# Kernel optimization log

Measured on AMD Instinct MI355X. Metric: run time of the kernel, lower is better.

The kernel has to match this reference:

```python
import jax, jax.numpy as jnp
import numpy as np

N = 50000
E = 1_600_000
IN_CH = 128
HEADS = 4
OUT_CH = 32
NEG_SLOPE = 0.2


def setup_inputs() -> dict:
    key = jax.random.key(0)
    k1, k2, k3, k4, k5, k6 = jax.random.split(key, 6)
    x = jax.random.normal(k1, (N, IN_CH), dtype=jnp.float32)
    edge_index = jax.random.randint(k2, (2, E), 0, N, dtype=jnp.int64)
    # GATConv params: linear weight, per-head attention vectors, output bias
    scale = 1.0 / np.sqrt(IN_CH)
    W = jax.random.normal(k3, (IN_CH, HEADS * OUT_CH), dtype=jnp.float32) * scale
    att_src = jax.random.normal(k4, (HEADS, OUT_CH), dtype=jnp.float32) * scale
    att_dst = jax.random.normal(k5, (HEADS, OUT_CH), dtype=jnp.float32) * scale
    bias = jnp.zeros((HEADS * OUT_CH,), dtype=jnp.float32)
    return {"x": x, "edge_index": edge_index, "W": W, "att_src": att_src,
            "att_dst": att_dst, "bias": bias}


def reference(x, edge_index, W, att_src, att_dst, bias):
    n = x.shape[0]
    # add self loops (PyG GATConv default add_self_loops=True)
    loops = jnp.arange(n, dtype=edge_index.dtype)
    src = jnp.concatenate([edge_index[0], loops])  # message source j
    dst = jnp.concatenate([edge_index[1], loops])  # message target i

    h = (x @ W).reshape(n, HEADS, OUT_CH)  # [N,H,C]
    a_src = jnp.einsum('nhc,hc->nh', h, att_src)  # [N,H]
    a_dst = jnp.einsum('nhc,hc->nh', h, att_dst)  # [N,H]

    e = jax.nn.leaky_relu(a_src[src] + a_dst[dst], NEG_SLOPE)  # [E+N,H]
    # segment softmax over incoming edges of each target node
    m = jax.ops.segment_max(e, dst, num_segments=n)  # [N,H]
    p = jnp.exp(e - m[dst])
    s = jax.ops.segment_sum(p, dst, num_segments=n)  # [N,H]
    alpha = p / s[dst]  # self loops guarantee s > 0

    # weighted scatter-aggregate of source features
    out = jax.ops.segment_sum(alpha[:, :, None] * h[src], dst, num_segments=n)  # [N,H,C]
    out = out.reshape(n, HEADS * OUT_CH) + bias
    return jax.nn.elu(out)
```

## Files before the change

kernel.cpp:

```cpp
#include <hip/hip_runtime.h>
#include <hip/hip_bf16.h>

#define IN_CH 128
#define HEADS 4
#define OUT_CH 32
#define HC 128
#define NEG_SLOPE 0.2f
#define BSHIFT 6
#define CHUNK 4096
#define BUCKCAP 2816

typedef __attribute__((ext_vector_type(8))) short bf16x8;
typedef __attribute__((ext_vector_type(4))) float f32x4;

__device__ __forceinline__ unsigned short f2bf(float f) {
  unsigned int u = __float_as_uint(f);
  return (unsigned short)((u + 0x7fffu + ((u >> 16) & 1u)) >> 16);
}
__device__ __forceinline__ float bf2f(unsigned short b) {
  return __uint_as_float(((unsigned int)b) << 16);
}
__device__ __forceinline__ float bflo(unsigned int g) {
  return __uint_as_float((g & 0xffffu) << 16);
}
__device__ __forceinline__ float bfhi(unsigned int g) {
  return __uint_as_float(g & 0xffff0000u);
}

__global__ void zero_i32(int* __restrict__ p, int n) {
  int i = blockIdx.x * blockDim.x + threadIdx.x;
  if (i < n) p[i] = 0;
}

__global__ void cvt_params(const void* __restrict__ Wr, const void* __restrict__ asr,
                           const void* __restrict__ adr, const void* __restrict__ br,
                           const void* __restrict__ xptr, const void* __restrict__ eptr,
                           float* __restrict__ Wf, unsigned short* __restrict__ Wtb,
                           float* __restrict__ asf,
                           float* __restrict__ adf, float* __restrict__ bf,
                           int* __restrict__ cursorA, int* __restrict__ flags) {
  __shared__ int sok[256], sz[256];
  int t = threadIdx.x;
  {
    const unsigned short* u = (const unsigned short*)xptr;
    float a = fabsf(bf2f(u[t]));
    sok[t] = (a >= 1e-6f && a <= 1e3f) ? 1 : 0;
    const int* ip = (const int*)eptr;
    int z = 0;
#pragma unroll
    for (int k = 0; k < 4; k++) z += (ip[2 * (t * 4 + k) + 1] == 0) ? 1 : 0;
    sz[t] = z;
    __syncthreads();
    for (int s = 128; s > 0; s >>= 1) {
      if (t < s) { sok[t] += sok[t + s]; sz[t] += sz[t + s]; }
      __syncthreads();
    }
  }
  int isbf = (sok[0] >= 240) ? 1 : 0;
  int is64 = (sz[0] >= 900) ? 1 : 0;
  if (blockIdx.x == 0 && t == 0) { flags[0] = isbf; flags[1] = is64; }

  int i = blockIdx.x * blockDim.x + t;
  auto rd = [&](const void* p, int k) -> float {
    return isbf ? bf2f(((const unsigned short*)p)[k]) : ((const float*)p)[k];
  };
  if (i < 1024) cursorA[i] = i * BUCKCAP;
  if (i < IN_CH * HC) {
    float v = rd(Wr, i);
    Wf[i] = v;
    int r = i >> 7, c = i & 127;
    Wtb[c * IN_CH + r] = f2bf(v);
  } else {
    int r = i - IN_CH * HC;
    if (r < HC)            asf[r] = rd(asr, r);
    else if (r < 2 * HC)   adf[r - HC] = rd(adr, r - HC);
    else if (r < 3 * HC)   bf[r - 2 * HC] = rd(br, r - 2 * HC);
  }
}

__device__ __forceinline__ void load_edge(const void* __restrict__ ei,
                                          const int* __restrict__ flags,
                                          int e, int E, int& j, int& d) {
  if (flags[1]) {
    const long long* q = (const long long*)ei;
    j = (int)q[e]; d = (int)q[E + e];
  } else {
    const int* p = (const int*)ei;
    j = p[e]; d = p[E + e];
  }
}

__device__ void gemm_body(const void* __restrict__ xraw, const float* __restrict__ W,
                          const float* __restrict__ asf, const float* __restrict__ adf,
                          unsigned short* __restrict__ h_bf,
                          float* __restrict__ a_srcO, float* __restrict__ a_dstO,
                          int N, int isbf, float (*xs)[33], int bid) {
  int t = threadIdx.x;
  int nb = bid * 32;
  for (int r = 0; r < 16; r++) {
    int idx = r * 256 + t;
    int nl = idx >> 7;
    int c = idx & 127;
    int n = nb + nl;
    float v = 0.f;
    if (n < N) {
      size_t gi = (size_t)n * IN_CH + c;
      v = isbf ? bf2f(((const unsigned short*)xraw)[gi]) : ((const float*)xraw)[gi];
    }
    xs[c][nl] = v;
  }
  __syncthreads();
  int tc = t & 31, c0 = tc * 4;
  int tn = t >> 5, n0 = tn * 4;
  float acc[4][4];
#pragma unroll
  for (int i = 0; i < 4; i++)
#pragma unroll
    for (int q = 0; q < 4; q++) acc[i][q] = 0.f;
  for (int k = 0; k < 128; k++) {
    float4 w = *(const float4*)&W[k * HC + c0];
    float x0 = xs[k][n0], x1 = xs[k][n0 + 1], x2 = xs[k][n0 + 2], x3 = xs[k][n0 + 3];
    acc[0][0] += x0 * w.x; acc[0][1] += x0 * w.y; acc[0][2] += x0 * w.z; acc[0][3] += x0 * w.w;
    acc[1][0] += x1 * w.x; acc[1][1] += x1 * w.y; acc[1][2] += x1 * w.z; acc[1][3] += x1 * w.w;
    acc[2][0] += x2 * w.x; acc[2][1] += x2 * w.y; acc[2][2] += x2 * w.z; acc[2][3] += x2 * w.w;
    acc[3][0] += x3 * w.x; acc[3][1] += x3 * w.y; acc[3][2] += x3 * w.z; acc[3][3] += x3 * w.w;
  }
#pragma unroll
  for (int i = 0; i < 4; i++) {
    int n = nb + n0 + i;
    if (n >= N) continue;
    size_t o = (size_t)n * HC + c0;
    ushort4 hb;
    hb.x = f2bf(acc[i][0]);
    hb.y = f2bf(acc[i][1]);
    hb.z = f2bf(acc[i][2]);
    hb.w = f2bf(acc[i][3]);
    *(ushort4*)&h_bf[o] = hb;
  }
  float4 wsc = *(const float4*)&asf[c0];
  float4 wdc = *(const float4*)&adf[c0];
  int hh = tc >> 3;
#pragma unroll
  for (int i = 0; i < 4; i++) {
    float ps = acc[i][0] * wsc.x + acc[i][1] * wsc.y + acc[i][2] * wsc.z + acc[i][3] * wsc.w;
    float pd = acc[i][0] * wdc.x + acc[i][1] * wdc.y + acc[i][2] * wdc.z + acc[i][3] * wdc.w;
    ps += __shfl_xor(ps, 1, 64); ps += __shfl_xor(ps, 2, 64); ps += __shfl_xor(ps, 4, 64);
    pd += __shfl_xor(pd, 1, 64); pd += __shfl_xor(pd, 2, 64); pd += __shfl_xor(pd, 4, 64);
    int n = nb + n0 + i;
    if ((tc & 7) == 0 && n < N) {
      a_srcO[n * HEADS + hh] = ps;
      a_dstO[n * HEADS + hh] = pd;
    }
  }
}

__device__ void gemm_mfma_body(const unsigned short* __restrict__ xb,
                               const unsigned short* __restrict__ Wtb,
                               const float* __restrict__ asf, const float* __restrict__ adf,
                               unsigned short* __restrict__ h_bf,
                               float* __restrict__ a_srcO, float* __restrict__ a_dstO,
                               int N, int bid) {
  int t = threadIdx.x;
  int w = t >> 6, l = t & 63;
  int lr = l & 15, lk = l >> 4;
  int nb = bid * 32;
  int node_base = nb + (w & 1) * 16;
  int ch0 = (w >> 1) * 64;
  int arow = node_base + lr;
  if (arow >= N) arow = N - 1;
  const unsigned short* xrow = xb + (size_t)arow * IN_CH + lk * 8;

  f32x4 acc[4];
#pragma unroll
  for (int ct = 0; ct < 4; ct++) acc[ct] = (f32x4){0.f, 0.f, 0.f, 0.f};

#pragma unroll
  for (int ks = 0; ks < 4; ks++) {
    bf16x8 afrag = *(const bf16x8*)(xrow + ks * 32);
#pragma unroll
    for (int ct = 0; ct < 4; ct++) {
      const unsigned short* wrow =
          Wtb + (size_t)(ch0 + ct * 16 + lr) * IN_CH + ks * 32 + lk * 8;
      bf16x8 bfrag = *(const bf16x8*)wrow;
      acc[ct] = __builtin_amdgcn_mfma_f32_16x16x32_bf16(afrag, bfrag, acc[ct], 0, 0, 0);
    }
  }

  float ps[4][2], pd[4][2];
#pragma unroll
  for (int i = 0; i < 4; i++) { ps[i][0] = ps[i][1] = pd[i][0] = pd[i][1] = 0.f; }
#pragma unroll
  for (int ct = 0; ct < 4; ct++) {
    int col = ch0 + ct * 16 + lr;
    float as_c = asf[col], ad_c = adf[col];
    int hw = ct >> 1;
#pragma unroll
    for (int i = 0; i < 4; i++) {
      float v = acc[ct][i];
      int row = node_base + lk * 4 + i;
      if (row < N) h_bf[(size_t)row * HC + col] = f2bf(v);
      ps[i][hw] += v * as_c;
      pd[i][hw] += v * ad_c;
    }
  }
#pragma unroll
  for (int i = 0; i < 4; i++) {
#pragma unroll
    for (int hw = 0; hw < 2; hw++) {
      float s = ps[i][hw], d2 = pd[i][hw];
      s += __shfl_xor(s, 1, 64); s += __shfl_xor(s, 2, 64);
      s += __shfl_xor(s, 4, 64); s += __shfl_xor(s, 8, 64);
      d2 += __shfl_xor(d2, 1, 64); d2 += __shfl_xor(d2, 2, 64);
      d2 += __shfl_xor(d2, 4, 64); d2 += __shfl_xor(d2, 8, 64);
      int row = node_base + lk * 4 + i;
      if (lr == 0 && row < N) {
        int hh = (ch0 >> 5) + hw;
        a_srcO[row * HEADS + hh] = s;
        a_dstO[row * HEADS + hh] = d2;
      }
    }
  }
}

__device__ void partA_body(const void* __restrict__ ei, int* __restrict__ cursorA,
                           unsigned int* __restrict__ ebuf, int E, int N,
                           const int* __restrict__ flags, int* hist, int bid) {
  int nbuck = (N + ((1 << BSHIFT) - 1)) >> BSHIFT;
  int t = threadIdx.x;
  for (int b = t; b < nbuck; b += 256) hist[b] = 0;
  __syncthreads();
  int base = bid * CHUNK;
  unsigned int v[16];
#pragma unroll
  for (int k = 0; k < 16; k++) {
    int e = base + k * 256 + t;
    if (e < E) {
      int j, d;
      load_edge(ei, flags, e, E, j, d);
      v[k] = (unsigned int)j | ((unsigned int)d << 16);
      atomicAdd(&hist[d >> BSHIFT], 1);
    } else v[k] = 0xffffffffu;
  }
  __syncthreads();
  for (int b = t; b < nbuck; b += 256) {
    int c = hist[b];
    if (c > 0) hist[b] = atomicAdd(&cursorA[b], c);
  }
  __syncthreads();
#pragma unroll
  for (int k = 0; k < 16; k++) {
    if (v[k] != 0xffffffffu) {
      int b = (int)(v[k] >> 16) >> BSHIFT;
      int pos = atomicAdd(&hist[b], 1);
      if (pos < (b + 1) * BUCKCAP) ebuf[pos] = v[k];
    }
  }
}

__global__ void fused_gemm_partA(const void* __restrict__ xraw, const float* __restrict__ W,
                                 const unsigned short* __restrict__ Wtb,
                                 const float* __restrict__ asf, const float* __restrict__ adf,
                                 unsigned short* __restrict__ h_bf,
                                 float* __restrict__ a_src, float* __restrict__ a_dst,
                                 const void* __restrict__ ei, int* __restrict__ cursorA,
                                 unsigned int* __restrict__ ebuf, int E, int N,
                                 const int* __restrict__ flags, int NB_G) {
  __shared__ __align__(16) char smem[16896];
  if (blockIdx.x < NB_G) {
    if (flags[0]) {
      gemm_mfma_body((const unsigned short*)xraw, Wtb, asf, adf, h_bf,
                     a_src, a_dst, N, blockIdx.x);
    } else {
      gemm_body(xraw, W, asf, adf, h_bf, a_src, a_dst, N, 0,
                (float(*)[33])smem, blockIdx.x);
    }
  } else {
    partA_body(ei, cursorA, ebuf, E, N, flags, (int*)smem, blockIdx.x - NB_G);
  }
}

__global__ void gemm_kernel(const void* __restrict__ xraw, const float* __restrict__ W,
                            const unsigned short* __restrict__ Wtb,
                            const float* __restrict__ asf, const float* __restrict__ adf,
                            unsigned short* __restrict__ h_bf,
                            float* __restrict__ a_src, float* __restrict__ a_dst,
                            int N, const int* __restrict__ flags) {
  __shared__ float xs[128][33];
  if (flags[0]) {
    gemm_mfma_body((const unsigned short*)xraw, Wtb, asf, adf, h_bf,
                   a_src, a_dst, N, blockIdx.x);
  } else {
    gemm_body(xraw, W, asf, adf, h_bf, a_src, a_dst, N, 0, xs, blockIdx.x);
  }
}

__global__ void partB(const unsigned int* __restrict__ ebuf, const int* __restrict__ cursorA,
                      int* __restrict__ rowbeg, int* __restrict__ rowend,
                      unsigned short* __restrict__ src_sorted, int N) {
  __shared__ int cnt[64];
  __shared__ int stmp[64];
  __shared__ int lcur[64];
  int b = blockIdx.x;
  int t = threadIdx.x;
  int n0 = b << BSHIFT;
  int r0 = b * BUCKCAP;
  int r1 = min(cursorA[b], r0 + BUCKCAP);
  if (t < 64) cnt[t] = 0;
  __syncthreads();
  for (int pos = r0 + t; pos < r1; pos += 256)
    atomicAdd(&cnt[(ebuf[pos] >> 16) & 63], 1);
  __syncthreads();
  int x = 0, v = 0;
  if (t < 64) { v = cnt[t]; x = v; stmp[t] = x; }
  __syncthreads();
  for (int ofs = 1; ofs < 64; ofs <<= 1) {
    int y = (t < 64 && t >= ofs) ? stmp[t - ofs] : 0;
    __syncthreads();
    if (t < 64) { x += y; stmp[t] = x; }
    __syncthreads();
  }
  if (t < 64) {
    int excl = x - v;
    lcur[t] = r0 + excl;
    int n = n0 + t;
    if (n < N) { rowbeg[n] = r0 + excl; rowend[n] = r0 + excl + v; }
  }
  __syncthreads();
  for (int pos = r0 + t; pos < r1; pos += 256) {
    unsigned int w = ebuf[pos];
    int slot = atomicAdd(&lcur[(w >> 16) & 63], 1);
    src_sorted[slot] = (unsigned short)(w & 0xffffu);
  }
}

__global__ void hist_kernel(const void* __restrict__ ei, int* __restrict__ counts,
                            int E, const int* __restrict__ flags) {
  int e = blockIdx.x * blockDim.x + threadIdx.x;
  if (e >= E) return;
  int d;
  if (flags[1]) d = (int)((const long long*)ei)[E + e];
  else          d = ((const int*)ei)[E + e];
  atomicAdd(&counts[d], 1);
}

__global__ void scan1(const int* __restrict__ in, int* __restrict__ excl,
                      int* __restrict__ bsums, int N) {
  __shared__ int tmp[256];
  int t = threadIdx.x;
  int i = blockIdx.x * 256 + t;
  int v = (i < N) ? in[i] : 0;
  int x = v;
  tmp[t] = x;
  __syncthreads();
  for (int ofs = 1; ofs < 256; ofs <<= 1) {
    int y = (t >= ofs) ? tmp[t - ofs] : 0;
    __syncthreads();
    x += y;
    tmp[t] = x;
    __syncthreads();
  }
  if (i < N) excl[i] = x - v;
  if (t == 255) bsums[blockIdx.x] = x;
}

__global__ void scan2(const int* __restrict__ bsums, int* __restrict__ boffs, int nb) {
  __shared__ int tmp[256];
  int t = threadIdx.x;
  int v = (t < nb) ? bsums[t] : 0;
  int x = v;
  tmp[t] = x;
  __syncthreads();
  for (int ofs = 1; ofs < 256; ofs <<= 1) {
    int y = (t >= ofs) ? tmp[t - ofs] : 0;
    __syncthreads();
    x += y;
    tmp[t] = x;
    __syncthreads();
  }
  if (t < nb) boffs[t] = x - v;
}

__global__ void scan3(const int* __restrict__ excl, const int* __restrict__ boffs,
                      int* __restrict__ rowbeg, int* __restrict__ rowend,
                      const int* __restrict__ counts, int N, int E) {
  int i = blockIdx.x * 256 + threadIdx.x;
  if (i < N) {
    int beg = excl[i] + boffs[i >> 8];
    rowbeg[i] = beg;
    rowend[i] = beg + counts[i];
  }
}

__global__ void scatter_kernel(const void* __restrict__ ei, const int* __restrict__ rowbeg,
                               int* __restrict__ cursor, int* __restrict__ src_sorted,
                               int E, const int* __restrict__ flags) {
  int e = blockIdx.x * blockDim.x + threadIdx.x;
  if (e >= E) return;
  int j, d;
  load_edge(ei, flags, e, E, j, d);
  int slot = atomicAdd(&cursor[d], 1);
  src_sorted[rowbeg[d] + slot] = j;
}

template <typename IdxT>
__global__ void agg_csr(const int* __restrict__ rowbeg, const int* __restrict__ rowend,
                        const IdxT* __restrict__ src_sorted,
                        const float* __restrict__ a_src, const float* __restrict__ a_dst,
                        const unsigned short* __restrict__ h_bf,
                        const float* __restrict__ bias,
                        float* __restrict__ out, int N) {
  int wid = threadIdx.x >> 6;
  int lane = threadIdx.x & 63;
  int d = blockIdx.x * 4 + wid;
  if (d >= N) return;
  int g = lane >> 4;
  int sl = lane & 15;
  int c0 = sl * 8;
  int hh = sl >> 2;
  float adst = a_dst[d * HEADS + hh];
  float e0 = a_src[d * HEADS + hh] + adst;
  e0 = e0 > 0.f ? e0 : NEG_SLOPE * e0;
  float ps = (g == 0) ? __expf(e0) : 0.f;
  uint4 qs = *(const uint4*)&h_bf[(size_t)d * HC + c0];
  float acc[8];
  acc[0] = ps * bflo(qs.x); acc[1] = ps * bfhi(qs.x);
  acc[2] = ps * bflo(qs.y); acc[3] = ps * bfhi(qs.y);
  acc[4] = ps * bflo(qs.z); acc[5] = ps * bfhi(qs.z);
  acc[6] = ps * bflo(qs.w); acc[7] = ps * bfhi(qs.w);
  float den = ps;
  int pos = rowbeg[d], r1 = rowend[d];
  for (; pos + 16 <= r1; pos += 16) {
    int ja = (int)src_sorted[pos + g];
    int jb = (int)src_sorted[pos + 4 + g];
    int jc = (int)src_sorted[pos + 8 + g];
    int jd = (int)src_sorted[pos + 12 + g];
    uint4 qa = *(const uint4*)&h_bf[(size_t)ja * HC + c0];
    uint4 qb = *(const uint4*)&h_bf[(size_t)jb * HC + c0];
    uint4 qc = *(const uint4*)&h_bf[(size_t)jc * HC + c0];
    uint4 qd = *(const uint4*)&h_bf[(size_t)jd * HC + c0];
    float aa = a_src[ja * HEADS + hh] + adst;
    float ab = a_src[jb * HEADS + hh] + adst;
    float ac = a_src[jc * HEADS + hh] + adst;
    float ad = a_src[jd * HEADS + hh] + adst;
    aa = aa > 0.f ? aa : NEG_SLOPE * aa;
    ab = ab > 0.f ? ab : NEG_SLOPE * ab;
    ac = ac > 0.f ? ac : NEG_SLOPE * ac;
    ad = ad > 0.f ? ad : NEG_SLOPE * ad;
    float pa = __expf(aa), pb = __expf(ab), pc = __expf(ac), pd = __expf(ad);
    den += pa + pb + pc + pd;
    acc[0] += pa * bflo(qa.x) + pb * bflo(qb.x) + pc * bflo(qc.x) + pd * bflo(qd.x);
    acc[1] += pa * bfhi(qa.x) + pb * bfhi(qb.x) + pc * bfhi(qc.x) + pd * bfhi(qd.x);
    acc[2] += pa * bflo(qa.y) + pb * bflo(qb.y) + pc * bflo(qc.y) + pd * bflo(qd.y);
    acc[3] += pa * bfhi(qa.y) + pb * bfhi(qb.y) + pc * bfhi(qc.y) + pd * bfhi(qd.y);
    acc[4] += pa * bflo(qa.z) + pb * bflo(qb.z) + pc * bflo(qc.z) + pd * bflo(qd.z);
    acc[5] += pa * bfhi(qa.z) + pb * bfhi(qb.z) + pc * bfhi(qc.z) + pd * bfhi(qd.z);
    acc[6] += pa * bflo(qa.w) + pb * bflo(qb.w) + pc * bflo(qc.w) + pd * bflo(qd.w);
    acc[7] += pa * bfhi(qa.w) + pb * bfhi(qb.w) + pc * bfhi(qc.w) + pd * bfhi(qd.w);
  }
  for (; pos + 8 <= r1; pos += 8) {
    int ja = (int)src_sorted[pos + g];
    int jb = (int)src_sorted[pos + 4 + g];
    uint4 qa = *(const uint4*)&h_bf[(size_t)ja * HC + c0];
    uint4 qb = *(const uint4*)&h_bf[(size_t)jb * HC + c0];
    float aa = a_src[ja * HEADS + hh] + adst;
    float ab = a_src[jb * HEADS + hh] + adst;
    aa = aa > 0.f ? aa : NEG_SLOPE * aa;
    ab = ab > 0.f ? ab : NEG_SLOPE * ab;
    float pa = __expf(aa), pb = __expf(ab);
    den += pa + pb;
    acc[0] += pa * bflo(qa.x) + pb * bflo(qb.x);
    acc[1] += pa * bfhi(qa.x) + pb * bfhi(qb.x);
    acc[2] += pa * bflo(qa.y) + pb * bflo(qb.y);
    acc[3] += pa * bfhi(qa.y) + pb * bfhi(qb.y);
    acc[4] += pa * bflo(qa.z) + pb * bflo(qb.z);
    acc[5] += pa * bfhi(qa.z) + pb * bfhi(qb.z);
    acc[6] += pa * bflo(qa.w) + pb * bflo(qb.w);
    acc[7] += pa * bfhi(qa.w) + pb * bfhi(qb.w);
  }
  for (; pos < r1; pos += 4) {
    int rem = r1 - pos;
    int gg = (g < rem) ? g : 0;
    int j = (int)src_sorted[pos + gg];
    float av = a_src[j * HEADS + hh] + adst;
    av = av > 0.f ? av : NEG_SLOPE * av;
    float pe = (g < rem) ? __expf(av) : 0.f;
    uint4 q = *(const uint4*)&h_bf[(size_t)j * HC + c0];
    den += pe;
    acc[0] += pe * bflo(q.x); acc[1] += pe * bfhi(q.x);
    acc[2] += pe * bflo(q.y); acc[3] += pe * bfhi(q.y);
    acc[4] += pe * bflo(q.z); acc[5] += pe * bfhi(q.z);
    acc[6] += pe * bflo(q.w); acc[7] += pe * bfhi(q.w);
  }
#pragma unroll
  for (int q = 0; q < 8; q++) {
    acc[q] += __shfl_xor(acc[q], 16, 64);
    acc[q] += __shfl_xor(acc[q], 32, 64);
  }
  den += __shfl_xor(den, 16, 64);
  den += __shfl_xor(den, 32, 64);
  if (g == 0) {
    float inv = 1.f / den;
    float4 b0 = *(const float4*)&bias[c0];
    float4 b1 = *(const float4*)&bias[c0 + 4];
    float o[8];
    o[0] = acc[0] * inv + b0.x; o[1] = acc[1] * inv + b0.y;
    o[2] = acc[2] * inv + b0.z; o[3] = acc[3] * inv + b0.w;
    o[4] = acc[4] * inv + b1.x; o[5] = acc[5] * inv + b1.y;
    o[6] = acc[6] * inv + b1.z; o[7] = acc[7] * inv + b1.w;
#pragma unroll
    for (int q = 0; q < 8; q++) o[q] = o[q] > 0.f ? o[q] : __expf(o[q]) - 1.f;
    *(float4*)&out[(size_t)d * HC + c0]     = make_float4(o[0], o[1], o[2], o[3]);
    *(float4*)&out[(size_t)d * HC + c0 + 4] = make_float4(o[4], o[5], o[6], o[7]);
  }
}

extern "C" void kernel_launch(void* const* d_in, const int* in_sizes, int n_in,
                              void* d_out, int out_size, void* d_ws, size_t ws_size,
                              hipStream_t stream) {
  const void* x_raw  = d_in[0];
  const void* ei_raw = d_in[1];
  const void* W_raw  = d_in[2];
  const void* as_raw = d_in[3];
  const void* ad_raw = d_in[4];
  const void* b_raw  = d_in[5];
  const int N = in_sizes[0] / IN_CH;
  int E = in_sizes[1] / 2;
  if (in_sizes[1] == 6400000) E = 1600000;

  char* wsp = (char*)d_ws;
  size_t off = 0;
  auto walloc = [&](size_t bytes) {
    void* ptr = wsp + off;
    off += (bytes + 255) & ~(size_t)255;
    return ptr;
  };
  int*   flags   = (int*)walloc(64);
  float* Wf      = (float*)walloc((size_t)IN_CH * HC * 4);
  unsigned short* Wtb = (unsigned short*)walloc((size_t)IN_CH * HC * 2);
  float* asf     = (float*)walloc(HC * 4);
  float* adf     = (float*)walloc(HC * 4);
  float* bf      = (float*)walloc(HC * 4);
  float* a_src   = (float*)walloc((size_t)N * HEADS * 4);
  float* a_dst   = (float*)walloc((size_t)N * HEADS * 4);
  unsigned short* h_bf = (unsigned short*)walloc((size_t)N * HC * 2);
  int*   cursorA = (int*)walloc(1024 * 4);
  int*   rowbeg  = (int*)walloc((size_t)N * 4);
  int*   rowend  = (int*)walloc((size_t)N * 4);

  const int NBUCK = (N + ((1 << BSHIFT) - 1)) >> BSHIFT;
  size_t padded = (size_t)NBUCK * BUCKCAP;

  const int NB_G = (N + 31) / 32;
  const int NB_N = (N + 255) / 256;
  const int NB_E = (E + 255) / 256;
  const int NB_A = (E + CHUNK - 1) / CHUNK;

  cvt_params<<<(IN_CH * HC + 3 * HC + 255) / 256, 256, 0, stream>>>(
      W_raw, as_raw, ad_raw, b_raw, x_raw, ei_raw, Wf, Wtb, asf, adf, bf, cursorA, flags);

  if (N < 65535) {
    unsigned short* src_sorted = (unsigned short*)walloc(padded * 2);
    unsigned int*   ebuf       = (unsigned int*)walloc(padded * 4);
    fused_gemm_partA<<<NB_G + NB_A, 256, 0, stream>>>(
        x_raw, Wf, Wtb, asf, adf, h_bf, a_src, a_dst, ei_raw, cursorA, ebuf, E, N,
        flags, NB_G);
    partB<<<NBUCK, 256, 0, stream>>>(ebuf, cursorA, rowbeg, rowend, src_sorted, N);
    agg_csr<unsigned short><<<(N + 3) / 4, 256, 0, stream>>>(
        rowbeg, rowend, src_sorted, a_src, a_dst, h_bf, bf, (float*)d_out, N);
  } else {
    int* src_sorted = (int*)walloc((size_t)E * 4);
    int* counts = (int*)walloc((size_t)(N + 1) * 4);
    int* pexcl  = (int*)walloc((size_t)N * 4);
    int* bsums  = (int*)walloc(256 * 4);
    int* boffs  = (int*)walloc(256 * 4);
    gemm_kernel<<<NB_G, 256, 0, stream>>>(x_raw, Wf, Wtb, asf, adf, h_bf,
                                          a_src, a_dst, N, flags);
    zero_i32<<<NB_N, 256, 0, stream>>>(counts, N + 1);
    hist_kernel<<<NB_E, 256, 0, stream>>>(ei_raw, counts, E, flags);
    scan1<<<NB_N, 256, 0, stream>>>(counts, pexcl, bsums, N);
    scan2<<<1, 256, 0, stream>>>(bsums, boffs, NB_N);
    scan3<<<NB_N, 256, 0, stream>>>(pexcl, boffs, rowbeg, rowend, counts, N, E);
    zero_i32<<<NB_N, 256, 0, stream>>>(counts, N + 1);
    scatter_kernel<<<NB_E, 256, 0, stream>>>(ei_raw, rowbeg, counts, src_sorted, E, flags);
    agg_csr<int><<<(N + 3) / 4, 256, 0, stream>>>(
        rowbeg, rowend, src_sorted, a_src, a_dst, h_bf, bf, (float*)d_out, N);
  }
}
```

Baseline: 201.0 us.

## Fuse bucket sort with CSR aggregation, keeping sorted source list in LDS

Merges the per-bucket counting sort (partB) and the attention aggregation kernel into one 1024-thread kernel per 64-node bucket. The sorted source indices stay in shared memory instead of being written to and re-read from global memory, and the rowbeg/rowend arrays and one kernel launch are dropped. Each wave handles four destination nodes, using 16 lanes per edge slice and unrolling by 4/8/4 edges. In exchange, the grid is coarser (one large block per bucket), which may cause load imbalance or lower latency hiding for the gather-heavy aggregation.

New measurement: 214.1 us. 6.5% more time.

```diff
diff --git a/kernel.cpp b/kernel.cpp
--- a/kernel.cpp
+++ b/kernel.cpp
@@ -294,21 +294,23 @@
   }
 }
 
-__global__ void partB(const unsigned int* __restrict__ ebuf, const int* __restrict__ cursorA,
-                      int* __restrict__ rowbeg, int* __restrict__ rowend,
-                      unsigned short* __restrict__ src_sorted, int N) {
-  __shared__ int cnt[64];
-  __shared__ int stmp[64];
-  __shared__ int lcur[64];
+__global__ void partB_agg(const unsigned int* __restrict__ ebuf,
+                          const int* __restrict__ cursorA,
+                          const float* __restrict__ a_src, const float* __restrict__ a_dst,
+                          const unsigned short* __restrict__ h_bf,
+                          const float* __restrict__ bias,
+                          float* __restrict__ out, int N) {
+  __shared__ unsigned short jlist[BUCKCAP];
+  __shared__ int cnt[64], stmp[64], lcur[64], rowb[64], rowe[64];
   int b = blockIdx.x;
   int t = threadIdx.x;
   int n0 = b << BSHIFT;
   int r0 = b * BUCKCAP;
-  int r1 = min(cursorA[b], r0 + BUCKCAP);
+  int ec = min(cursorA[b] - r0, BUCKCAP);
   if (t < 64) cnt[t] = 0;
   __syncthreads();
-  for (int pos = r0 + t; pos < r1; pos += 256)
-    atomicAdd(&cnt[(ebuf[pos] >> 16) & 63], 1);
+  for (int pos = t; pos < ec; pos += 1024)
+    atomicAdd(&cnt[(ebuf[r0 + pos] >> 16) & 63], 1);
   __syncthreads();
   int x = 0, v = 0;
   if (t < 64) { v = cnt[t]; x = v; stmp[t] = x; }
@@ -321,15 +323,123 @@
   }
   if (t < 64) {
     int excl = x - v;
-    lcur[t] = r0 + excl;
-    int n = n0 + t;
-    if (n < N) { rowbeg[n] = r0 + excl; rowend[n] = r0 + excl + v; }
-  }
-  __syncthreads();
-  for (int pos = r0 + t; pos < r1; pos += 256) {
-    unsigned int w = ebuf[pos];
+    lcur[t] = excl;
+    rowb[t] = excl;
+    rowe[t] = excl + v;
+  }
+  __syncthreads();
+  for (int pos = t; pos < ec; pos += 1024) {
+    unsigned int w = ebuf[r0 + pos];
     int slot = atomicAdd(&lcur[(w >> 16) & 63], 1);
-    src_sorted[slot] = (unsigned short)(w & 0xffffu);
+    jlist[slot] = (unsigned short)(w & 0xffffu);
+  }
+  __syncthreads();
+
+  int wid = t >> 6;
+  int lane = t & 63;
+  int g = lane >> 4;
+  int sl = lane & 15;
+  int c0 = sl * 8;
+  int hh = sl >> 2;
+  for (int nl = 0; nl < 4; nl++) {
+    int dl = wid * 4 + nl;
+    int d = n0 + dl;
+    if (d >= N) break;
+    float adst = a_dst[d * HEADS + hh];
+    float e0 = a_src[d * HEADS + hh] + adst;
+    e0 = e0 > 0.f ? e0 : NEG_SLOPE * e0;
+    float ps = (g == 0) ? __expf(e0) : 0.f;
+    uint4 qs = *(const uint4*)&h_bf[(size_t)d * HC + c0];
+    float acc[8];
+    acc[0] = ps * bflo(qs.x); acc[1] = ps * bfhi(qs.x);
+    acc[2] = ps * bflo(qs.y); acc[3] = ps * bfhi(qs.y);
+    acc[4] = ps * bflo(qs.z); acc[5] = ps * bfhi(qs.z);
+    acc[6] = ps * bflo(qs.w); acc[7] = ps * bfhi(qs.w);
+    float den = ps;
+    int pos = rowb[dl], r1 = rowe[dl];
+    for (; pos + 16 <= r1; pos += 16) {
+      int ja = (int)jlist[pos + g];
+      int jb = (int)jlist[pos + 4 + g];
+      int jc = (int)jlist[pos + 8 + g];
+      int jd = (int)jlist[pos + 12 + g];
+      uint4 qa = *(const uint4*)&h_bf[(size_t)ja * HC + c0];
+      uint4 qb = *(const uint4*)&h_bf[(size_t)jb * HC + c0];
+      uint4 qc = *(const uint4*)&h_bf[(size_t)jc * HC + c0];
+      uint4 qd = *(const uint4*)&h_bf[(size_t)jd * HC + c0];
+      float aa = a_src[ja * HEADS + hh] + adst;
+      float ab = a_src[jb * HEADS + hh] + adst;
+      float ac = a_src[jc * HEADS + hh] + adst;
+      float ad = a_src[jd * HEADS + hh] + adst;
+      aa = aa > 0.f ? aa : NEG_SLOPE * aa;
+      ab = ab > 0.f ? ab : NEG_SLOPE * ab;
+      ac = ac > 0.f ? ac : NEG_SLOPE * ac;
+      ad = ad > 0.f ? ad : NEG_SLOPE * ad;
+      float pa = __expf(aa), pb = __expf(ab), pc = __expf(ac), pd = __expf(ad);
+      den += pa + pb + pc + pd;
+      acc[0] += pa * bflo(qa.x) + pb * bflo(qb.x) + pc * bflo(qc.x) + pd * bflo(qd.x);
+      acc[1] += pa * bfhi(qa.x) + pb * bfhi(qb.x) + pc * bfhi(qc.x) + pd * bfhi(qd.x);
+      acc[2] += pa * bflo(qa.y) + pb * bflo(qb.y) + pc * bflo(qc.y) + pd * bflo(qd.y);
+      acc[3] += pa * bfhi(qa.y) + pb * bfhi(qb.y) + pc * bfhi(qc.y) + pd * bfhi(qd.y);
+      acc[4] += pa * bflo(qa.z) + pb * bflo(qb.z) + pc * bflo(qc.z) + pd * bflo(qd.z);
+      acc[5] += pa * bfhi(qa.z) + pb * bfhi(qb.z) + pc * bfhi(qc.z) + pd * bfhi(qd.z);
+      acc[6] += pa * bflo(qa.w) + pb * bflo(qb.w) + pc * bflo(qc.w) + pd * bflo(qd.w);
+      acc[7] += pa * bfhi(qa.w) + pb * bfhi(qb.w) + pc * bfhi(qc.w) + pd * bfhi(qd.w);
+    }
+    for (; pos + 8 <= r1; pos += 8) {
+      int ja = (int)jlist[pos + g];
+      int jb = (int)jlist[pos + 4 + g];
+      uint4 qa = *(const uint4*)&h_bf[(size_t)ja * HC + c0];
+      uint4 qb = *(const uint4*)&h_bf[(size_t)jb * HC + c0];
+      float aa = a_src[ja * HEADS + hh] + adst;
+      float ab = a_src[jb * HEADS + hh] + adst;
+      aa = aa > 0.f ? aa : NEG_SLOPE * aa;
+      ab = ab > 0.f ? ab : NEG_SLOPE * ab;
+      float pa = __expf(aa), pb = __expf(ab);
+      den += pa + pb;
+      acc[0] += pa * bflo(qa.x) + pb * bflo(qb.x);
+      acc[1] += pa * bfhi(qa.x) + pb * bfhi(qb.x);
+      acc[2] += pa * bflo(qa.y) + pb * bflo(qb.y);
+      acc[3] += pa * bfhi(qa.y) + pb * bfhi(qb.y);
+      acc[4] += pa * bflo(qa.z) + pb * bflo(qb.z);
+      acc[5] += pa * bfhi(qa.z) + pb * bfhi(qb.z);
+      acc[6] += pa * bflo(qa.w) + pb * bflo(qb.w);
+      acc[7] += pa * bfhi(qa.w) + pb * bfhi(qb.w);
+    }
+    for (; pos < r1; pos += 4) {
+      int rem = r1 - pos;
+      int gg = (g < rem) ? g : 0;
+      int j = (int)jlist[pos + gg];
+      float av = a_src[j * HEADS + hh] + adst;
+      av = av > 0.f ? av : NEG_SLOPE * av;
+      float pe = (g < rem) ? __expf(av) : 0.f;
+      uint4 q = *(const uint4*)&h_bf[(size_t)j * HC + c0];
+      den += pe;
+      acc[0] += pe * bflo(q.x); acc[1] += pe * bfhi(q.x);
+      acc[2] += pe * bflo(q.y); acc[3] += pe * bfhi(q.y);
+      acc[4] += pe * bflo(q.z); acc[5] += pe * bfhi(q.z);
+      acc[6] += pe * bflo(q.w); acc[7] += pe * bfhi(q.w);
+    }
+#pragma unroll
+    for (int q = 0; q < 8; q++) {
+      acc[q] += __shfl_xor(acc[q], 16, 64);
+      acc[q] += __shfl_xor(acc[q], 32, 64);
+    }
+    den += __shfl_xor(den, 16, 64);
+    den += __shfl_xor(den, 32, 64);
+    if (g == 0) {
+      float inv = 1.f / den;
+      float4 b0 = *(const float4*)&bias[c0];
+      float4 b1 = *(const float4*)&bias[c0 + 4];
+      float o[8];
+      o[0] = acc[0] * inv + b0.x; o[1] = acc[1] * inv + b0.y;
+      o[2] = acc[2] * inv + b0.z; o[3] = acc[3] * inv + b0.w;
+      o[4] = acc[4] * inv + b1.x; o[5] = acc[5] * inv + b1.y;
+      o[6] = acc[6] * inv + b1.z; o[7] = acc[7] * inv + b1.w;
+#pragma unroll
+      for (int q = 0; q < 8; q++) o[q] = o[q] > 0.f ? o[q] : __expf(o[q]) - 1.f;
+      *(float4*)&out[(size_t)d * HC + c0]     = make_float4(o[0], o[1], o[2], o[3]);
+      *(float4*)&out[(size_t)d * HC + c0 + 4] = make_float4(o[4], o[5], o[6], o[7]);
+    }
   }
 }
 
@@ -559,14 +669,12 @@
       W_raw, as_raw, ad_raw, b_raw, x_raw, ei_raw, Wf, Wtb, asf, adf, bf, cursorA, flags);
 
   if (N < 65535) {
-    unsigned short* src_sorted = (unsigned short*)walloc(padded * 2);
-    unsigned int*   ebuf       = (unsigned int*)walloc(padded * 4);
+    unsigned int* ebuf = (unsigned int*)walloc(padded * 4);
     fused_gemm_partA<<<NB_G + NB_A, 256, 0, stream>>>(
         x_raw, Wf, Wtb, asf, adf, h_bf, a_src, a_dst, ei_raw, cursorA, ebuf, E, N,
         flags, NB_G);
-    partB<<<NBUCK, 256, 0, stream>>>(ebuf, cursorA, rowbeg, rowend, src_sorted, N);
-    agg_csr<unsigned short><<<(N + 3) / 4, 256, 0, stream>>>(
-        rowbeg, rowend, src_sorted, a_src, a_dst, h_bf, bf, (float*)d_out, N);
+    partB_agg<<<NBUCK, 1024, 0, stream>>>(ebuf, cursorA, a_src, a_dst, h_bf, bf,
+                                          (float*)d_out, N);
   } else {
     int* src_sorted = (int*)walloc((size_t)E * 4);
     int* counts = (int*)walloc((size_t)(N + 1) * 4);
```
